# Performance work log

Measured on AMD Instinct MI355X. Metric: run time of the kernel, lower is better.

Reference implementation:

```python
import jax, jax.numpy as jnp
import numpy as np

B, L, EMBED = 8, 4096, 1024
HEADS, WIN, SHIFT = 16, 128, 64
HD = EMBED // HEADS
MLP_HIDDEN = 4 * EMBED
SCALE = HD ** -0.5
NW = L // WIN


def _layer_norm(x, w, b, eps=1e-5):
    m = x.mean(-1, keepdims=True)
    v = x.var(-1, keepdims=True)
    return (x - m) * jax.lax.rsqrt(v + eps) * w + b


def _compute_mask():
    # replicate SwinBlock1D._compute_mask: region ids over full L, then windowed
    sizes = [L - WIN, WIN - SHIFT, SHIFT]
    region = np.zeros(L, np.int32)
    pos = 0
    for i, s in enumerate(sizes):
        region[pos:pos + s] = i
        pos += s
    region = region.reshape(NW, WIN)
    diff = region[:, None, :] - region[:, :, None]  # (nW, W, W)
    return jnp.asarray(np.where(diff != 0, -100.0, 0.0).astype(np.float32))


_MASK = _compute_mask()
_REL_IDX = jnp.arange(WIN)[None, :] - jnp.arange(WIN)[:, None] + WIN - 1  # (W, W)


def setup_inputs() -> dict:
    key = jax.random.key(0)
    ks = jax.random.split(key, 8)
    s = 0.02

    def w(k, shape):
        return jax.random.normal(k, shape, jnp.float32) * s

    return {
        "x": jax.random.normal(ks[0], (B, L, EMBED), jnp.float32),
        "qkv_w": w(ks[1], (3 * EMBED, EMBED)),
        "qkv_b": jnp.zeros((3 * EMBED,), jnp.float32),
        "proj_w": w(ks[2], (EMBED, EMBED)),
        "proj_b": jnp.zeros((EMBED,), jnp.float32),
        "rpb": w(ks[3], (2 * WIN - 1, HEADS)),
        "norm1_w": jnp.ones((EMBED,), jnp.float32),
        "norm1_b": jnp.zeros((EMBED,), jnp.float32),
        "norm2_w": jnp.ones((EMBED,), jnp.float32),
        "norm2_b": jnp.zeros((EMBED,), jnp.float32),
        "mlp_w1": w(ks[4], (MLP_HIDDEN, EMBED)),
        "mlp_b1": jnp.zeros((MLP_HIDDEN,), jnp.float32),
        "mlp_w2": w(ks[5], (EMBED, MLP_HIDDEN)),
        "mlp_b2": jnp.zeros((EMBED,), jnp.float32),
    }


def reference(x, qkv_w, qkv_b, proj_w, proj_b, rpb,
              norm1_w, norm1_b, norm2_w, norm2_b,
              mlp_w1, mlp_b1, mlp_w2, mlp_b2):
    BW = B * NW
    shortcut = x
    h = _layer_norm(x, norm1_w, norm1_b)
    # shifted-window attention (shift_size > 0)
    h = jnp.roll(h, -SHIFT, axis=1)
    win = h.reshape(BW, WIN, EMBED)
    qkv = (win @ qkv_w.T + qkv_b).reshape(BW, WIN, 3, HEADS, HD)
    qkv = qkv.transpose(2, 0, 3, 1, 4)  # (3, BW, H, W, hd)
    q, k, v = qkv[0], qkv[1], qkv[2]
    attn = jnp.einsum('bhqd,bhkd->bhqk', q, k) * SCALE
    bias = rpb[_REL_IDX]  # (W, W, H)
    attn = attn + bias.transpose(2, 0, 1)[None]
    attn = attn.reshape(B, NW, HEADS, WIN, WIN) + _MASK[None, :, None]
    attn = jax.nn.softmax(attn.reshape(BW, HEADS, WIN, WIN), axis=-1)
    # dropout layers are identity in eval mode
    out = jnp.einsum('bhqk,bhkd->bhqd', attn, v)
    out = out.transpose(0, 2, 1, 3).reshape(BW, WIN, EMBED)
    out = out @ proj_w.T + proj_b
    out = out.reshape(B, L, EMBED)
    out = jnp.roll(out, SHIFT, axis=1)
    x = shortcut + out
    # MLP block
    h2 = _layer_norm(x, norm2_w, norm2_b)
    h2 = jax.nn.gelu(h2 @ mlp_w1.T + mlp_b1, approximate=False) @ mlp_w2.T + mlp_b2
    return x + h2
```

## Files before the change

### kernel.cpp

```cpp
#include <hip/hip_runtime.h>
#include <cstdint>
#include <cstddef>

#define SEQ_L   4096
#define EMBED   1024
#define HEADS   16
#define WINSZ   128
#define SHIFTSZ 64
#define HD      64
#define NWIN    32
#define MTOT    32768
#define ATT_SCALE 0.125f

typedef __bf16 bf16x8 __attribute__((ext_vector_type(8)));
typedef float  f32x4  __attribute__((ext_vector_type(4)));

typedef __attribute__((address_space(3))) void       lds_void;
typedef const __attribute__((address_space(1))) void gbl_void;

#define GLDS16(g, s) __builtin_amdgcn_global_load_lds((gbl_void*)(g), (lds_void*)(s), 16, 0, 0)

__device__ __forceinline__ unsigned short f2bf(float f) {
    unsigned int u = __float_as_uint(f);
    u += 0x7fffu + ((u >> 16) & 1u);
    return (unsigned short)(u >> 16);
}

__launch_bounds__(256)
__global__ void wconv4(const float* __restrict__ s0, const float* __restrict__ s1,
                       const float* __restrict__ s2, const float* __restrict__ s3,
                       unsigned short* __restrict__ d0, unsigned short* __restrict__ d1,
                       unsigned short* __restrict__ d2, unsigned short* __restrict__ d3)
{
    const int b = blockIdx.x;
    const float* s; unsigned short* d; int off;
    if (b < 3072)      { s = s0; d = d0; off = b; }
    else if (b < 4096) { s = s1; d = d1; off = b - 3072; }
    else if (b < 8192) { s = s2; d = d2; off = b - 4096; }
    else               { s = s3; d = d3; off = b - 8192; }
    const int i = (off * 256 + threadIdx.x) * 4;
    const float4 v = *(const float4*)(s + i);
    ushort4 o;
    o.x = f2bf(v.x); o.y = f2bf(v.y); o.z = f2bf(v.z); o.w = f2bf(v.w);
    *(ushort4*)(d + i) = o;
}

__launch_bounds__(256)
__global__ void ln_kernel(const float* __restrict__ x, const float* __restrict__ gw,
                          const float* __restrict__ gb, unsigned short* __restrict__ out,
                          int shift)
{
    const int row  = blockIdx.x * 4 + (threadIdx.x >> 6);
    const int lane = threadIdx.x & 63;
    const int b    = row >> 12;
    const int lw   = row & 4095;
    const int src  = (b << 12) | ((lw + shift) & 4095);
    const float* xr = x + (size_t)src * EMBED;

    float4 v[4];
    float s = 0.f, q = 0.f;
#pragma unroll
    for (int j = 0; j < 4; ++j) {
        v[j] = ((const float4*)xr)[lane + j * 64];
        s += v[j].x + v[j].y + v[j].z + v[j].w;
        q += v[j].x * v[j].x + v[j].y * v[j].y + v[j].z * v[j].z + v[j].w * v[j].w;
    }
#pragma unroll
    for (int off = 32; off > 0; off >>= 1) {
        s += __shfl_xor(s, off);
        q += __shfl_xor(q, off);
    }
    const float mean = s * (1.0f / 1024.0f);
    const float rstd = rsqrtf(q * (1.0f / 1024.0f) - mean * mean + 1e-5f);

    unsigned short* orow = out + (size_t)row * EMBED;
#pragma unroll
    for (int j = 0; j < 4; ++j) {
        const float4 w4 = ((const float4*)gw)[lane + j * 64];
        const float4 b4 = ((const float4*)gb)[lane + j * 64];
        ushort4 o;
        o.x = f2bf((v[j].x - mean) * rstd * w4.x + b4.x);
        o.y = f2bf((v[j].y - mean) * rstd * w4.y + b4.y);
        o.z = f2bf((v[j].z - mean) * rstd * w4.z + b4.z);
        o.w = f2bf((v[j].w - mean) * rstd * w4.w + b4.w);
        ((ushort4*)orow)[lane + j * 64] = o;
    }
}

__device__ __forceinline__ void stage_half(const unsigned short* __restrict__ g, int ldk,
                                           char* ldsbase, int tid)
{
    const int r  = tid >> 3;
    const int cg = ((tid & 7) ^ (r & 7)) << 3;
    GLDS16(g + (size_t)r        * ldk + cg, ldsbase + tid * 16);
    GLDS16(g + (size_t)(r + 64) * ldk + cg, ldsbase + 8192 + tid * 16);
}

__device__ __forceinline__ bf16x8 lds_frag(const char* half, int row, int koff)
{
    const int off = koff ^ ((row & 7) << 4);
    return *(const bf16x8*)(half + row * 128 + off);
}

template<int EPI>
__launch_bounds__(512, 2)
__global__ void gemm256(const unsigned short* __restrict__ A, const unsigned short* __restrict__ W,
                        const float* __restrict__ bias, void* __restrict__ outv,
                        const float* __restrict__ resid, int M, int N, int K)
{
    __shared__ __align__(16) char lds[131072];
    const int tid = threadIdx.x;
    const int l   = tid & 63, w = tid >> 6;
    const int wm  = w >> 2, wn = w & 3;
    const int lr  = l & 15, hi = l >> 4;
    const int k0off = hi << 4;
    const int br0   = (wn & 1) << 6;

    int id = blockIdx.x;
    const int nwg = gridDim.x;
    id = (id & 7) * (nwg >> 3) + (id >> 3);
    const int Ntl = N >> 8;
    const int m0  = (id / Ntl) << 8;
    const int n0  = (id % Ntl) << 8;
    const int NT  = K >> 6;

#define HTB(b, ab, h) (lds + ((((b) << 1 | (ab)) << 1 | (h)) << 14))

    stage_half(A + (size_t)m0         * K, K, HTB(0,0,0), tid);
    stage_half(A + (size_t)(m0 + 128) * K, K, HTB(0,0,1), tid);
    stage_half(W + (size_t)n0         * K, K, HTB(0,1,0), tid);
    stage_half(W + (size_t)(n0 + 128) * K, K, HTB(0,1,1), tid);
    asm volatile("s_waitcnt vmcnt(0)" ::: "memory");
    __builtin_amdgcn_s_barrier();

    f32x4 acc[8][4];
#pragma unroll
    for (int f = 0; f < 8; ++f)
#pragma unroll
        for (int n = 0; n < 4; ++n)
            acc[f][n] = (f32x4){0.f, 0.f, 0.f, 0.f};

    bf16x8 bf[4][2], af0[2][2], af1[2][2];

#define LOAD_A_BANK(bank, AHP, F0)                                          \
    af##bank[0][0] = lds_frag(AHP, (F0) * 16 + lr,      k0off);             \
    af##bank[0][1] = lds_frag(AHP, (F0) * 16 + lr,      64 + k0off);        \
    af##bank[1][0] = lds_frag(AHP, (F0) * 16 + 16 + lr, k0off);             \
    af##bank[1][1] = lds_frag(AHP, (F0) * 16 + 16 + lr, 64 + k0off);

#define MFMA_BANK(bank, F0)                                                 \
    __builtin_amdgcn_s_setprio(1);                                          \
    _Pragma("unroll")                                                       \
    for (int n = 0; n < 4; ++n) {                                           \
        acc[F0][n]       = __builtin_amdgcn_mfma_f32_16x16x32_bf16(af##bank[0][0], bf[n][0], acc[F0][n], 0, 0, 0);       \
        acc[F0][n]       = __builtin_amdgcn_mfma_f32_16x16x32_bf16(af##bank[0][1], bf[n][1], acc[F0][n], 0, 0, 0);       \
        acc[(F0) + 1][n] = __builtin_amdgcn_mfma_f32_16x16x32_bf16(af##bank[1][0], bf[n][0], acc[(F0) + 1][n], 0, 0, 0); \
        acc[(F0) + 1][n] = __builtin_amdgcn_mfma_f32_16x16x32_bf16(af##bank[1][1], bf[n][1], acc[(F0) + 1][n], 0, 0, 0); \
    }                                                                       \
    __builtin_amdgcn_s_setprio(0);

#define TILE(BUF)                                                              \
    {                                                                          \
        const char* Ah = HTB(BUF, 0, wm);                                      \
        const char* Bh = HTB(BUF, 1, wn >> 1);                                 \
        _Pragma("unroll")                                                      \
        for (int n = 0; n < 4; ++n) {                                          \
            bf[n][0] = lds_frag(Bh, br0 + n * 16 + lr, k0off);                 \
            bf[n][1] = lds_frag(Bh, br0 + n * 16 + lr, 64 + k0off);            \
        }                                                                      \
        LOAD_A_BANK(0, Ah, 0)                                                  \
        if (t + 1 < NT) {                                                      \
            const unsigned short* An = A + (size_t)m0 * K + (size_t)(t + 1) * 64; \
            const unsigned short* Wn = W + (size_t)n0 * K + (size_t)(t + 1) * 64; \
            stage_half(An,                   K, HTB(BUF ^ 1, 0, 0), tid);      \
            stage_half(An + (size_t)128 * K, K, HTB(BUF ^ 1, 0, 1), tid);      \
            stage_half(Wn,                   K, HTB(BUF ^ 1, 1, 0), tid);      \
            stage_half(Wn + (size_t)128 * K, K, HTB(BUF ^ 1, 1, 1), tid);      \
        }                                                                      \
        LOAD_A_BANK(1, Ah, 2)                                                  \
        asm volatile("s_waitcnt lgkmcnt(4)" ::: "memory");                     \
        MFMA_BANK(0, 0)                                                        \
        LOAD_A_BANK(0, Ah, 4)                                                  \
        asm volatile("s_waitcnt lgkmcnt(4)" ::: "memory");                     \
        MFMA_BANK(1, 2)                                                        \
        LOAD_A_BANK(1, Ah, 6)                                                  \
        asm volatile("s_waitcnt lgkmcnt(4)" ::: "memory");                     \
        MFMA_BANK(0, 4)                                                        \
        asm volatile("s_waitcnt lgkmcnt(0)" ::: "memory");                     \
        MFMA_BANK(1, 6)                                                        \
        asm volatile("s_waitcnt vmcnt(0)" ::: "memory");                       \
        __builtin_amdgcn_s_barrier();                                          \
    }

    int t;
    for (int u = 0; u < (NT >> 1); ++u) {
        t = 2 * u;     TILE(0)
        t = 2 * u + 1; TILE(1)
    }
#undef TILE
#undef LOAD_A_BANK
#undef MFMA_BANK
#undef HTB

    const int cb = n0 + wn * 64;
    float bv[4];
#pragma unroll
    for (int n = 0; n < 4; ++n) bv[n] = bias[cb + n * 16 + lr];

#pragma unroll
    for (int f = 0; f < 8; ++f) {
        const int mbase = m0 + wm * 128 + f * 16 + hi * 4;
#pragma unroll
        for (int n = 0; n < 4; ++n) {
            const int col = cb + n * 16 + lr;
#pragma unroll
            for (int r = 0; r < 4; ++r) {
                const int m = mbase + r;
                float v = acc[f][n][r] + bv[n];
                if constexpr (EPI == 0) {
                    ((unsigned short*)outv)[(size_t)m * N + col] = f2bf(v);
                } else if constexpr (EPI == 1) {
                    const int bb = m >> 12;
                    const int lw = m & 4095;
                    const int ll = (lw + SHIFTSZ) & 4095;
                    const size_t di = ((size_t)(bb << 12) + ll) * (size_t)N + col;
                    ((float*)outv)[di] = resid[di] + v;
                } else if constexpr (EPI == 2) {
                    const float g = 0.5f * v * (1.0f + erff(v * 0.70710678118654752f));
                    ((unsigned short*)outv)[(size_t)m * N + col] = f2bf(g);
                } else {
                    float* o = (float*)outv;
                    const size_t di = (size_t)m * N + col;
                    o[di] = o[di] + v;
                }
            }
        }
    }
}

#define SM_VT  34816
#define SM_RPB 52224

__device__ __forceinline__ bf16x8 vt_frag(const char* vt, int d, int kbyte)
{
    const int key = ((d >> 3) & 7) << 4;
    return *(const bf16x8*)(vt + d * 272 + (kbyte ^ key));
}

__launch_bounds__(256, 3)
__global__ void attn_kernel(const unsigned short* __restrict__ qkv, const float* __restrict__ rpb,
                            unsigned short* __restrict__ outp)
{
    __shared__ __align__(16) char smem[53248];

    const int t   = threadIdx.x;
    const int l   = t & 63;
    const int w   = t >> 6;
    const int lr  = l & 15;
    const int lq  = l >> 4;
    const int lk  = lq * 8;
    const int blk = blockIdx.x;
    const int win = blk >> 4;
    const int h   = blk & 15;
    const bool masked = ((win & (NWIN - 1)) == NWIN - 1);

    const unsigned short* qb = qkv + (size_t)(win * WINSZ) * (3 * EMBED) + h * HD;
    const unsigned short* kb = qb + EMBED;
    const unsigned short* vb = qb + 2 * EMBED;
    const int mrow = w * 32;
    float* rpbl = (float*)(smem + SM_RPB);

    bf16x8 aqr[2][2];
#pragma unroll
    for (int ks = 0; ks < 2; ++ks)
#pragma unroll
        for (int mi = 0; mi < 2; ++mi)
            aqr[ks][mi] = *(const bf16x8*)(qb + (size_t)(mrow + mi * 16 + lr) * (3 * EMBED) + ks * 32 + lk);

    if (t < 255) rpbl[t] = rpb[t * HEADS + h];

    {
        const int c = t & 7;
#pragma unroll
        for (int p = 0; p < 4; ++p) {
            const int r  = (t >> 3) + p * 32;
            const int cg = (c ^ (r & 7)) << 3;
            GLDS16(kb + (size_t)r * (3 * EMBED) + cg, smem + p * 4096 + t * 16);
        }
    }
    {
        const int c  = t & 7;
        const int tp = t >> 3;
        char* base = smem + SM_VT;
        const int key = c << 4;
#pragma unroll
        for (int p = 0; p < 2; ++p) {
            const int k0 = 2 * (tp + p * 32);
            const uint4 va = *(const uint4*)(vb + (size_t)k0       * (3 * EMBED) + c * 8);
            const uint4 vc = *(const uint4*)(vb + (size_t)(k0 + 1) * (3 * EMBED) + c * 8);
            const unsigned int ra[4] = {va.x, va.y, va.z, va.w};
            const unsigned int rc[4] = {vc.x, vc.y, vc.z, vc.w};
#pragma unroll
            for (int e2 = 0; e2 < 4; ++e2) {
                const int d0 = c * 8 + e2 * 2;
                const unsigned int w0 = (ra[e2] & 0xffffu) | ((rc[e2] & 0xffffu) << 16);
                const unsigned int w1 = (ra[e2] >> 16)     | (rc[e2] & 0xffff0000u);
                *(unsigned int*)(base + (size_t)d0       * 272 + ((2 * k0) ^ key)) = w0;
                *(unsigned int*)(base + (size_t)(d0 + 1) * 272 + ((2 * k0) ^ key)) = w1;
            }
        }
    }
    asm volatile("s_waitcnt vmcnt(0)" ::: "memory");
    __syncthreads();

    f32x4 sacc[2][8];
#pragma unroll
    for (int a = 0; a < 2; ++a)
#pragma unroll
        for (int b = 0; b < 8; ++b)
            sacc[a][b] = (f32x4){0.f, 0.f, 0.f, 0.f};

#pragma unroll
    for (int ks = 0; ks < 2; ++ks) {
        const int kby = ks * 64 + lq * 16;
        bf16x8 bk8[8];
#pragma unroll
        for (int ni = 0; ni < 8; ++ni)
            bk8[ni] = lds_frag(smem, ni * 16 + lr, kby);
#pragma unroll
        for (int mi = 0; mi < 2; ++mi)
#pragma unroll
            for (int ni = 0; ni < 8; ++ni)
                sacc[mi][ni] = __builtin_amdgcn_mfma_f32_16x16x32_bf16(aqr[ks][mi], bk8[ni], sacc[mi][ni], 0, 0, 0);
    }

    __syncthreads();

#pragma unroll
    for (int mi = 0; mi < 2; ++mi)
#pragma unroll
        for (int r = 0; r < 4; ++r) {
            const int i = mrow + mi * 16 + lq * 4 + r;
            float v[8];
            float mx = -1e30f;
#pragma unroll
            for (int ni = 0; ni < 8; ++ni) {
                const int j = ni * 16 + lr;
                float sv = sacc[mi][ni][r] * ATT_SCALE + rpbl[j - i + WINSZ - 1];
                if (masked && ((i >= SHIFTSZ) != (j >= SHIFTSZ))) sv -= 100.0f;
                v[ni] = sv;
                mx = fmaxf(mx, sv);
            }
#pragma unroll
            for (int s = 1; s < 16; s <<= 1) mx = fmaxf(mx, __shfl_xor(mx, s));
            float sm = 0.f;
#pragma unroll
            for (int ni = 0; ni < 8; ++ni) {
                const float p = __expf(v[ni] - mx);
                v[ni] = p;
                sm += p;
            }
#pragma unroll
            for (int s = 1; s < 16; s <<= 1) sm += __shfl_xor(sm, s);
            const float rs = 1.0f / sm;
#pragma unroll
            for (int ni = 0; ni < 8; ++ni)
                *(unsigned short*)(smem + ((size_t)i * 136 + ni * 16 + lr) * 2) = f2bf(v[ni] * rs);
        }

    __syncthreads();

    f32x4 oacc[2][4];
#pragma unroll
    for (int a = 0; a < 2; ++a)
#pragma unroll
        for (int b = 0; b < 4; ++b)
            oacc[a][b] = (f32x4){0.f, 0.f, 0.f, 0.f};

#pragma unroll
    for (int ks = 0; ks < 4; ++ks) {
        const int k0 = ks * 32;
        bf16x8 ap[2], av[4];
#pragma unroll
        for (int mi = 0; mi < 2; ++mi)
            ap[mi] = *(const bf16x8*)(smem + ((size_t)(mrow + mi * 16 + lr) * 136 + k0 + lk) * 2);
#pragma unroll
        for (int ni = 0; ni < 4; ++ni)
            av[ni] = vt_frag(smem + SM_VT, ni * 16 + lr, k0 * 2 + lq * 16);
#pragma unroll
        for (int mi = 0; mi < 2; ++mi)
#pragma unroll
            for (int ni = 0; ni < 4; ++ni)
                oacc[mi][ni] = __builtin_amdgcn_mfma_f32_16x16x32_bf16(ap[mi], av[ni], oacc[mi][ni], 0, 0, 0);
    }

    unsigned short* ob = outp + (size_t)(win * WINSZ) * EMBED + h * HD;
#pragma unroll
    for (int mi = 0; mi < 2; ++mi)
#pragma unroll
        for (int ni = 0; ni < 4; ++ni)
#pragma unroll
            for (int r = 0; r < 4; ++r) {
                const int i = mrow + mi * 16 + lq * 4 + r;
                const int d = ni * 16 + lr;
                ob[(size_t)i * EMBED + d] = f2bf(oacc[mi][ni][r]);
            }
}

extern "C" void kernel_launch(void* const* d_in, const int* in_sizes, int n_in,
                              void* d_out, int out_size, void* d_ws, size_t ws_size,
                              hipStream_t stream)
{
    const float* x      = (const float*)d_in[0];
    const float* qkv_w  = (const float*)d_in[1];
    const float* qkv_b  = (const float*)d_in[2];
    const float* proj_w = (const float*)d_in[3];
    const float* proj_b = (const float*)d_in[4];
    const float* rpb    = (const float*)d_in[5];
    const float* n1w    = (const float*)d_in[6];
    const float* n1b    = (const float*)d_in[7];
    const float* n2w    = (const float*)d_in[8];
    const float* n2b    = (const float*)d_in[9];
    const float* w1     = (const float*)d_in[10];
    const float* b1     = (const float*)d_in[11];
    const float* w2     = (const float*)d_in[12];
    const float* b2     = (const float*)d_in[13];
    float* out = (float*)d_out;

    unsigned short* wqkv  = (unsigned short*)d_ws;
    unsigned short* wproj = wqkv  + (size_t)3072 * 1024;
    unsigned short* wm1   = wproj + (size_t)1024 * 1024;
    unsigned short* wm2   = wm1   + (size_t)4096 * 1024;
    unsigned short* bufA  = wm2   + (size_t)4096 * 1024;
    unsigned short* bufB  = bufA  + (size_t)MTOT * EMBED;

    wconv4<<<12288, 256, 0, stream>>>(qkv_w, proj_w, w1, w2, wqkv, wproj, wm1, wm2);

    ln_kernel<<<8192, 256, 0, stream>>>(x, n1w, n1b, bufA, SHIFTSZ);

    gemm256<0><<<dim3(1536), 512, 0, stream>>>(bufA, wqkv, qkv_b, bufB, nullptr, MTOT, 3 * EMBED, EMBED);

    attn_kernel<<<4096, 256, 0, stream>>>(bufB, rpb, bufA);

    gemm256<1><<<dim3(512), 512, 0, stream>>>(bufA, wproj, proj_b, out, x, MTOT, EMBED, EMBED);

    ln_kernel<<<8192, 256, 0, stream>>>(out, n2w, n2b, bufA, 0);

    for (int c = 0; c < 2; ++c) {
        const size_t r0 = (size_t)c * 16384;
        gemm256<2><<<dim3(1024), 512, 0, stream>>>(bufA + r0 * EMBED, wm1, b1, bufB, nullptr,
                                                   16384, 4 * EMBED, EMBED);
        gemm256<3><<<dim3(256), 512, 0, stream>>>(bufB, wm2, b2, out + r0 * EMBED, nullptr,
                                                  16384, EMBED, 4 * EMBED);
    }
}
```

Measured before the change: 1.135 ms.

## Run MLP first GEMM in FP8 with scaled MFMA and fused GELU

Quantizes the LN2 output and the MLP up-projection weights (scaled by 64) to FP8 e4m3, and adds a new 256x256 GEMM kernel that uses the 16x16x128 f8f6f4 scaled MFMA with a fused bias+GELU epilogue that undoes the weight scale. This halves the bytes moved for that GEMM and doubles the MFMA throughput per instruction compared with bf16. In exchange it loses accuracy from FP8 rounding of activations and weights, which may exceed tolerance.

```diff
diff --git a/kernel.cpp b/kernel.cpp
--- a/kernel.cpp
+++ b/kernel.cpp
@@ -1,4 +1,5 @@
 #include <hip/hip_runtime.h>
+#include <hip/hip_fp8.h>
 #include <cstdint>
 #include <cstddef>
 
@@ -14,6 +15,8 @@
 
 typedef __bf16 bf16x8 __attribute__((ext_vector_type(8)));
 typedef float  f32x4  __attribute__((ext_vector_type(4)));
+typedef int    i32x4v __attribute__((ext_vector_type(4)));
+typedef int    i32x8v __attribute__((ext_vector_type(8)));
 
 typedef __attribute__((address_space(3))) void       lds_void;
 typedef const __attribute__((address_space(1))) void gbl_void;
@@ -26,28 +29,42 @@
     return (unsigned short)(u >> 16);
 }
 
+__device__ __forceinline__ unsigned char f2fp8(float f) {
+    __hip_fp8_e4m3 v(f);
+    return (unsigned char)v.__x;
+}
+
 __launch_bounds__(256)
 __global__ void wconv4(const float* __restrict__ s0, const float* __restrict__ s1,
                        const float* __restrict__ s2, const float* __restrict__ s3,
                        unsigned short* __restrict__ d0, unsigned short* __restrict__ d1,
-                       unsigned short* __restrict__ d2, unsigned short* __restrict__ d3)
+                       unsigned char* __restrict__ d2, unsigned short* __restrict__ d3)
 {
     const int b = blockIdx.x;
-    const float* s; unsigned short* d; int off;
-    if (b < 3072)      { s = s0; d = d0; off = b; }
-    else if (b < 4096) { s = s1; d = d1; off = b - 3072; }
-    else if (b < 8192) { s = s2; d = d2; off = b - 4096; }
-    else               { s = s3; d = d3; off = b - 8192; }
-    const int i = (off * 256 + threadIdx.x) * 4;
-    const float4 v = *(const float4*)(s + i);
-    ushort4 o;
-    o.x = f2bf(v.x); o.y = f2bf(v.y); o.z = f2bf(v.z); o.w = f2bf(v.w);
-    *(ushort4*)(d + i) = o;
-}
-
+    if (b >= 4096 && b < 8192) {
+        const int i = ((b - 4096) * 256 + threadIdx.x) * 4;
+        const float4 v = *(const float4*)(s2 + i);
+        uchar4 o;
+        o.x = f2fp8(v.x * 64.f); o.y = f2fp8(v.y * 64.f);
+        o.z = f2fp8(v.z * 64.f); o.w = f2fp8(v.w * 64.f);
+        *(uchar4*)(d2 + i) = o;
+    } else {
+        const float* s; unsigned short* d; int off;
+        if (b < 3072)      { s = s0; d = d0; off = b; }
+        else if (b < 4096) { s = s1; d = d1; off = b - 3072; }
+        else               { s = s3; d = d3; off = b - 8192; }
+        const int i = (off * 256 + threadIdx.x) * 4;
+        const float4 v = *(const float4*)(s + i);
+        ushort4 o;
+        o.x = f2bf(v.x); o.y = f2bf(v.y); o.z = f2bf(v.z); o.w = f2bf(v.w);
+        *(ushort4*)(d + i) = o;
+    }
+}
+
+template<int OUT8>
 __launch_bounds__(256)
 __global__ void ln_kernel(const float* __restrict__ x, const float* __restrict__ gw,
-                          const float* __restrict__ gb, unsigned short* __restrict__ out,
+                          const float* __restrict__ gb, void* __restrict__ outv,
                           int shift)
 {
     const int row  = blockIdx.x * 4 + (threadIdx.x >> 6);
@@ -73,17 +90,21 @@
     const float mean = s * (1.0f / 1024.0f);
     const float rstd = rsqrtf(q * (1.0f / 1024.0f) - mean * mean + 1e-5f);
 
-    unsigned short* orow = out + (size_t)row * EMBED;
 #pragma unroll
     for (int j = 0; j < 4; ++j) {
         const float4 w4 = ((const float4*)gw)[lane + j * 64];
         const float4 b4 = ((const float4*)gb)[lane + j * 64];
-        ushort4 o;
-        o.x = f2bf((v[j].x - mean) * rstd * w4.x + b4.x);
-        o.y = f2bf((v[j].y - mean) * rstd * w4.y + b4.y);
-        o.z = f2bf((v[j].z - mean) * rstd * w4.z + b4.z);
-        o.w = f2bf((v[j].w - mean) * rstd * w4.w + b4.w);
-        ((ushort4*)orow)[lane + j * 64] = o;
+        const float r0 = (v[j].x - mean) * rstd * w4.x + b4.x;
+        const float r1 = (v[j].y - mean) * rstd * w4.y + b4.y;
+        const float r2 = (v[j].z - mean) * rstd * w4.z + b4.z;
+        const float r3 = (v[j].w - mean) * rstd * w4.w + b4.w;
+        if constexpr (OUT8 == 0) {
+            ushort4 o; o.x = f2bf(r0); o.y = f2bf(r1); o.z = f2bf(r2); o.w = f2bf(r3);
+            ((ushort4*)((unsigned short*)outv + (size_t)row * EMBED))[lane + j * 64] = o;
+        } else {
+            uchar4 o; o.x = f2fp8(r0); o.y = f2fp8(r1); o.z = f2fp8(r2); o.w = f2fp8(r3);
+            ((uchar4*)((unsigned char*)outv + (size_t)row * EMBED))[lane + j * 64] = o;
+        }
     }
 }
 
@@ -225,14 +246,144 @@
                     const int ll = (lw + SHIFTSZ) & 4095;
                     const size_t di = ((size_t)(bb << 12) + ll) * (size_t)N + col;
                     ((float*)outv)[di] = resid[di] + v;
-                } else if constexpr (EPI == 2) {
-                    const float g = 0.5f * v * (1.0f + erff(v * 0.70710678118654752f));
-                    ((unsigned short*)outv)[(size_t)m * N + col] = f2bf(g);
                 } else {
                     float* o = (float*)outv;
                     const size_t di = (size_t)m * N + col;
                     o[di] = o[di] + v;
                 }
+            }
+        }
+    }
+}
+
+__device__ __forceinline__ void stage_half8(const unsigned char* __restrict__ g, int ldkB,
+                                            char* ldsbase, int tid)
+{
+    const int r  = tid >> 3;
+    const int cg = ((tid & 7) ^ (r & 7)) << 4;
+    GLDS16(g + (size_t)r        * ldkB + cg, ldsbase + tid * 16);
+    GLDS16(g + (size_t)(r + 64) * ldkB + cg, ldsbase + 8192 + tid * 16);
+}
+
+__device__ __forceinline__ i32x8v lds_frag8(const char* half, int row, int koff)
+{
+    const int key = (row & 7) << 4;
+    const i32x4v lo = *(const i32x4v*)(half + row * 128 + (koff ^ key));
+    const i32x4v hi = *(const i32x4v*)(half + row * 128 + ((koff + 16) ^ key));
+    i32x8v r = {lo[0], lo[1], lo[2], lo[3], hi[0], hi[1], hi[2], hi[3]};
+    return r;
+}
+
+__launch_bounds__(512, 2)
+__global__ void gemm256f8(const unsigned char* __restrict__ A, const unsigned char* __restrict__ W,
+                          const float* __restrict__ bias, unsigned short* __restrict__ outp,
+                          int M, int N, int K)
+{
+    __shared__ __align__(16) char lds[131072];
+    const int tid = threadIdx.x;
+    const int l   = tid & 63, w = tid >> 6;
+    const int wm  = w >> 2, wn = w & 3;
+    const int lr  = l & 15, hi = l >> 4;
+    const int kbase = hi << 5;
+    const int br0   = (wn & 1) << 6;
+
+    int id = blockIdx.x;
+    const int nwg = gridDim.x;
+    id = (id & 7) * (nwg >> 3) + (id >> 3);
+    const int Ntl = N >> 8;
+    const int m0  = (id / Ntl) << 8;
+    const int n0  = (id % Ntl) << 8;
+    const int NT  = K >> 7;
+
+#define HTB(b, ab, h) (lds + ((((b) << 1 | (ab)) << 1 | (h)) << 14))
+
+    stage_half8(A + (size_t)m0         * K, K, HTB(0,0,0), tid);
+    stage_half8(A + (size_t)(m0 + 128) * K, K, HTB(0,0,1), tid);
+    stage_half8(W + (size_t)n0         * K, K, HTB(0,1,0), tid);
+    stage_half8(W + (size_t)(n0 + 128) * K, K, HTB(0,1,1), tid);
+    asm volatile("s_waitcnt vmcnt(0)" ::: "memory");
+    __builtin_amdgcn_s_barrier();
+
+    f32x4 acc[8][4];
+#pragma unroll
+    for (int f = 0; f < 8; ++f)
+#pragma unroll
+        for (int n = 0; n < 4; ++n)
+            acc[f][n] = (f32x4){0.f, 0.f, 0.f, 0.f};
+
+    i32x8v bfr[4], af0[2], af1[2];
+
+#define LOAD_A8(bank, AHP, F0)                                              \
+    af##bank[0] = lds_frag8(AHP, (F0) * 16 + lr,      kbase);               \
+    af##bank[1] = lds_frag8(AHP, (F0) * 16 + 16 + lr, kbase);
+
+#define MFMA8(bank, F0)                                                     \
+    __builtin_amdgcn_s_setprio(1);                                          \
+    _Pragma("unroll")                                                       \
+    for (int n = 0; n < 4; ++n) {                                           \
+        acc[F0][n]       = __builtin_amdgcn_mfma_scale_f32_16x16x128_f8f6f4(af##bank[0], bfr[n], acc[F0][n],       0, 0, 0, 127, 0, 127); \
+        acc[(F0) + 1][n] = __builtin_amdgcn_mfma_scale_f32_16x16x128_f8f6f4(af##bank[1], bfr[n], acc[(F0) + 1][n], 0, 0, 0, 127, 0, 127); \
+    }                                                                       \
+    __builtin_amdgcn_s_setprio(0);
+
+#define TILE8(BUF)                                                             \
+    {                                                                          \
+        const char* Ah = HTB(BUF, 0, wm);                                      \
+        const char* Bh = HTB(BUF, 1, wn >> 1);                                 \
+        _Pragma("unroll")                                                      \
+        for (int n = 0; n < 4; ++n)                                            \
+            bfr[n] = lds_frag8(Bh, br0 + n * 16 + lr, kbase);                  \
+        LOAD_A8(0, Ah, 0)                                                      \
+        if (t + 1 < NT) {                                                      \
+            const unsigned char* An = A + (size_t)m0 * K + (size_t)(t + 1) * 128; \
+            const unsigned char* Wn = W + (size_t)n0 * K + (size_t)(t + 1) * 128; \
+            stage_half8(An,                   K, HTB(BUF ^ 1, 0, 0), tid);     \
+            stage_half8(An + (size_t)128 * K, K, HTB(BUF ^ 1, 0, 1), tid);     \
+            stage_half8(Wn,                   K, HTB(BUF ^ 1, 1, 0), tid);     \
+            stage_half8(Wn + (size_t)128 * K, K, HTB(BUF ^ 1, 1, 1), tid);     \
+        }                                                                      \
+        LOAD_A8(1, Ah, 2)                                                      \
+        asm volatile("s_waitcnt lgkmcnt(4)" ::: "memory");                     \
+        MFMA8(0, 0)                                                            \
+        LOAD_A8(0, Ah, 4)                                                      \
+        asm volatile("s_waitcnt lgkmcnt(4)" ::: "memory");                     \
+        MFMA8(1, 2)                                                            \
+        LOAD_A8(1, Ah, 6)                                                      \
+        asm volatile("s_waitcnt lgkmcnt(4)" ::: "memory");                     \
+        MFMA8(0, 4)                                                            \
+        asm volatile("s_waitcnt lgkmcnt(0)" ::: "memory");                     \
+        MFMA8(1, 6)                                                            \
+        asm volatile("s_waitcnt vmcnt(0)" ::: "memory");                       \
+        __builtin_amdgcn_s_barrier();                                          \
+    }
+
+    int t;
+    for (int u = 0; u < (NT >> 1); ++u) {
+        t = 2 * u;     TILE8(0)
+        t = 2 * u + 1; TILE8(1)
+    }
+#undef TILE8
+#undef LOAD_A8
+#undef MFMA8
+#undef HTB
+
+    const int cb = n0 + wn * 64;
+    float bv[4];
+#pragma unroll
+    for (int n = 0; n < 4; ++n) bv[n] = bias[cb + n * 16 + lr];
+
+#pragma unroll
+    for (int f = 0; f < 8; ++f) {
+        const int mbase = m0 + wm * 128 + f * 16 + hi * 4;
+#pragma unroll
+        for (int n = 0; n < 4; ++n) {
+            const int col = cb + n * 16 + lr;
+#pragma unroll
+            for (int r = 0; r < 4; ++r) {
+                const int m = mbase + r;
+                const float v = acc[f][n][r] * 0.015625f + bv[n];
+                const float g = 0.5f * v * (1.0f + erff(v * 0.70710678118654752f));
+                outp[(size_t)m * N + col] = f2bf(g);
             }
         }
     }
@@ -428,15 +579,15 @@
     float* out = (float*)d_out;
 
     unsigned short* wqkv  = (unsigned short*)d_ws;
-    unsigned short* wproj = wqkv  + (size_t)3072 * 1024;
-    unsigned short* wm1   = wproj + (size_t)1024 * 1024;
-    unsigned short* wm2   = wm1   + (size_t)4096 * 1024;
-    unsigned short* bufA  = wm2   + (size_t)4096 * 1024;
-    unsigned short* bufB  = bufA  + (size_t)MTOT * EMBED;
+    unsigned short* wproj = wqkv + (size_t)3072 * 1024;
+    unsigned char*  wm1   = (unsigned char*)(wproj + (size_t)1024 * 1024);
+    unsigned short* wm2   = (unsigned short*)(wm1 + (size_t)4096 * 1024);
+    unsigned short* bufA  = wm2 + (size_t)4096 * 1024;
+    unsigned short* bufB  = bufA + (size_t)MTOT * EMBED;
 
     wconv4<<<12288, 256, 0, stream>>>(qkv_w, proj_w, w1, w2, wqkv, wproj, wm1, wm2);
 
-    ln_kernel<<<8192, 256, 0, stream>>>(x, n1w, n1b, bufA, SHIFTSZ);
+    ln_kernel<0><<<8192, 256, 0, stream>>>(x, n1w, n1b, bufA, SHIFTSZ);
 
     gemm256<0><<<dim3(1536), 512, 0, stream>>>(bufA, wqkv, qkv_b, bufB, nullptr, MTOT, 3 * EMBED, EMBED);
 
@@ -444,12 +595,13 @@
 
     gemm256<1><<<dim3(512), 512, 0, stream>>>(bufA, wproj, proj_b, out, x, MTOT, EMBED, EMBED);
 
-    ln_kernel<<<8192, 256, 0, stream>>>(out, n2w, n2b, bufA, 0);
+    unsigned char* ln2o = (unsigned char*)bufA;
+    ln_kernel<1><<<8192, 256, 0, stream>>>(out, n2w, n2b, ln2o, 0);
 
     for (int c = 0; c < 2; ++c) {
         const size_t r0 = (size_t)c * 16384;
-        gemm256<2><<<dim3(1024), 512, 0, stream>>>(bufA + r0 * EMBED, wm1, b1, bufB, nullptr,
-                                                   16384, 4 * EMBED, EMBED);
+        gemm256f8<<<dim3(1024), 512, 0, stream>>>(ln2o + r0 * EMBED, wm1, b1, bufB,
+                                                  16384, 4 * EMBED, EMBED);
         gemm256<3><<<dim3(256), 512, 0, stream>>>(bufB, wm2, b2, out + r0 * EMBED, nullptr,
                                                   16384, EMBED, 4 * EMBED);
     }
```

New measurement: 1.354 ms. 19.3% more time.
